# Optimization experiments

Measured on AMD Instinct MI355X. Metric: run time of the kernel, lower is better.

Reference implementation:

```python
import jax, jax.numpy as jnp
import numpy as np

N_AGENTS = 32
STATE_DIM = 2048
EMBED = 64
BS, T = 64, 32


def setup_inputs() -> dict:
    key = jax.random.key(0)
    ks = jax.random.split(key, 12)
    def lin(k, fan_in, fan_out):
        return jax.random.normal(k, (fan_in, fan_out), dtype=jnp.float32) / np.sqrt(fan_in)
    return {
        "agent_qs": jax.random.normal(ks[0], (BS, T, N_AGENTS), dtype=jnp.float32),
        "states": jax.random.normal(ks[1], (BS, T, STATE_DIM), dtype=jnp.float32),
        "Ww1": lin(ks[2], STATE_DIM, EMBED * N_AGENTS),
        "bw1": jnp.zeros((EMBED * N_AGENTS,), jnp.float32),
        "Wwf": lin(ks[3], STATE_DIM, EMBED),
        "bwf": jnp.zeros((EMBED,), jnp.float32),
        "Wb1": lin(ks[4], STATE_DIM, EMBED),
        "bb1": jnp.zeros((EMBED,), jnp.float32),
        "Wv1": lin(ks[5], STATE_DIM, EMBED),
        "bv1": jnp.zeros((EMBED,), jnp.float32),
        "Wv2": lin(ks[6], EMBED, 1),
        "bv2": jnp.zeros((1,), jnp.float32),
    }


def _mix(qs, st, Ww1, bw1, Wwf, bwf, Wb1, bb1, Wv1, bv1, Wv2, bv2):
    # qs: [B,1,A], st: [B,S] -> q_tot [B]
    w1 = jnp.abs(st @ Ww1 + bw1).reshape(-1, N_AGENTS, EMBED)          # [B,A,E]
    b1 = (st @ Wb1 + bb1)[:, None, :]                                   # [B,1,E]
    hidden = jax.nn.elu(jnp.einsum('bia,bae->bie', qs, w1) + b1)        # [B,1,E]
    w_final = jnp.abs(st @ Wwf + bwf)                                   # [B,E]
    v = jax.nn.relu(st @ Wv1 + bv1) @ Wv2 + bv2                         # [B,1]
    y = jnp.einsum('bie,be->bi', hidden, w_final) + v                   # [B,1]
    return y[:, 0]


def reference(agent_qs, states, Ww1, bw1, Wwf, bwf, Wb1, bb1, Wv1, bv1, Wv2, bv2):
    bs = agent_qs.shape[0]
    st = states.reshape(-1, STATE_DIM)                   # [B,S]
    qs = agent_qs.reshape(-1, 1, N_AGENTS)               # [B,1,A]
    B = st.shape[0]
    params = (Ww1, bw1, Wwf, bwf, Wb1, bb1, Wv1, bv1, Wv2, bv2)

    # --- wc_calculate (fully detached) ---
    q_tot = _mix(qs, st, *params)                        # [B]
    dim2 = STATE_DIM // N_AGENTS
    st3 = st.reshape(B, N_AGENTS, dim2)
    mask = 1.0 - jnp.eye(N_AGENTS, dtype=st.dtype)       # [A,A]: row i zeros agent-i chunk
    masked = (st3[None, :, :, :] * mask[:, None, :, None]).reshape(N_AGENTS * B, STATE_DIM)
    qs_rep = jnp.broadcast_to(qs[None], (N_AGENTS, B, 1, N_AGENTS)).reshape(N_AGENTS * B, 1, N_AGENTS)
    q1 = _mix(qs_rep, masked, *params).reshape(N_AGENTS, B)
    wc = jnp.abs(q_tot[None, :] - q1).T                  # [B,A]
    wc = wc / jnp.maximum(jnp.linalg.norm(wc, axis=1, keepdims=True), 1e-12)
    wc = jax.lax.stop_gradient(wc)[:, None, :]           # [B,1,A]

    # --- final mix with importance-weighted qs ---
    q_tot_final = _mix(qs * wc, st, *params)             # [B]
    return q_tot_final.reshape(bs, -1, 1)
```

## Files before the change

### kernel.cpp

```cpp
#include <hip/hip_runtime.h>
#include <math.h>
#include <stdint.h>

#define NA 32
#define SD 2048
#define BT 2048
#define NFRG 144

typedef float floatx4 __attribute__((ext_vector_type(4)));
typedef short bf16x8  __attribute__((ext_vector_type(8)));

__device__ __forceinline__ unsigned short f2bf(float f) {
    union { float f; uint32_t u; } v; v.f = f;
    uint32_t r = v.u + 0x7FFFu + ((v.u >> 16) & 1u);
    return (unsigned short)(r >> 16);
}

__device__ __forceinline__ void stage16(const void* g, void* l) {
    __builtin_amdgcn_global_load_lds(
        (const __attribute__((address_space(1))) void*)g,
        (__attribute__((address_space(3))) void*)l,
        16, 0, 0);
}


__global__ __launch_bounds__(256) void k0_ast(const float* __restrict__ st,
                                              unsigned short* __restrict__ stA) {
    const int t  = threadIdx.x;
    const int kc = blockIdx.x * 4 + (t >> 6);
    const int bt = blockIdx.y;
    const int l  = t & 63;
    const int quad = l >> 4, l16 = l & 15;
    const float* src = st + (size_t)(bt * 16 + l16) * SD + kc * 32 + quad * 8;
    float4 v0 = *(const float4*)(src);
    float4 v1 = *(const float4*)(src + 4);
    ushort4 o0, o1;
    o0.x = f2bf(v0.x); o0.y = f2bf(v0.y); o0.z = f2bf(v0.z); o0.w = f2bf(v0.w);
    o1.x = f2bf(v1.x); o1.y = f2bf(v1.y); o1.z = f2bf(v1.z); o1.w = f2bf(v1.w);
    unsigned short* dst = stA + ((size_t)bt * 64 + kc) * 512 + l * 8;
    *(ushort4*)(dst)     = o0;
    *(ushort4*)(dst + 4) = o1;
}

__global__ __launch_bounds__(256) void k0_wswz(const float* __restrict__ Ww1,
                                               const float* __restrict__ Wwf,
                                               const float* __restrict__ Wb1,
                                               const float* __restrict__ Wv1,
                                               unsigned short* __restrict__ Wswz) {
    const int t = threadIdx.x;
    const int i = blockIdx.y;
    const int f = blockIdx.x * 2 + (t >> 7);
    const int h = (t >> 6) & 1;
    const int l = t & 63;
    const int quad = l >> 4, l16 = l & 15;
    const int n = f * 16 + l16;

    const float* src; int ld, nr = 0;
    if (f < 128)      { src = Ww1; ld = 2048; nr = n; }
    else if (f < 132) { src = Wwf; ld = 64;   nr = n - 2048; }
    else if (f < 136) { src = Wb1; ld = 64;   nr = n - 2112; }
    else if (f < 140) { src = Wv1; ld = 64;   nr = n - 2176; }
    else              { src = nullptr; ld = 64; }

    const int k0 = i * 64 + h * 32 + quad * 8;
    unsigned short vals[8];
    #pragma unroll
    for (int j = 0; j < 8; j++)
        vals[j] = src ? f2bf(src[(size_t)(k0 + j) * ld + nr]) : (unsigned short)0;

    unsigned short* dst = Wswz + (((size_t)i * NFRG + f) * 2 + h) * 512 + l * 8;
    ushort4 o0 = {vals[0], vals[1], vals[2], vals[3]};
    ushort4 o1 = {vals[4], vals[5], vals[6], vals[7]};
    *(ushort4*)(dst)     = o0;
    *(ushort4*)(dst + 4) = o1;
}

__global__ void k0_bias(const float* __restrict__ bw1, const float* __restrict__ bwf,
                        const float* __restrict__ bb1, const float* __restrict__ bv1,
                        float* __restrict__ bcat) {
    int n = blockIdx.x * 256 + threadIdx.x;
    if (n >= NFRG * 16) return;
    float v = 0.f;
    if (n < 2048)      v = bw1[n];
    else if (n < 2112) v = bwf[n - 2048];
    else if (n < 2176) v = bb1[n - 2112];
    else if (n < 2240) v = bv1[n - 2176];
    bcat[n] = v;
}

__global__ __launch_bounds__(256) void k1_gemm(const unsigned short* __restrict__ stA,
                                               const unsigned short* __restrict__ Wswz,
                                               const float* __restrict__ bcat,
                                               float* __restrict__ Ycn)
{
    const int t = threadIdx.x;
    const int m0t = blockIdx.x * 4;
    const int n0f = blockIdx.y * 8;
    const int wid = t >> 6, lane = t & 63;
    const int wm = wid & 1, wn = wid >> 1;
    const int l16 = lane & 15;

    floatx4 acc[2][4];
    #pragma unroll
    for (int i = 0; i < 2; i++)
        #pragma unroll
        for (int j = 0; j < 4; j++) acc[i][j] = (floatx4)0.f;

    const unsigned short* Ap0 = stA + ((size_t)(m0t + wm * 2 + 0) * 64) * 512 + lane * 8;
    const unsigned short* Ap1 = stA + ((size_t)(m0t + wm * 2 + 1) * 64) * 512 + lane * 8;
    const unsigned short* Bbase = Wswz + ((size_t)(n0f + wn * 4) * 2) * 512 + lane * 8;

    bf16x8 a0c = *(const bf16x8*)(Ap0);
    bf16x8 a1c = *(const bf16x8*)(Ap1);
    bf16x8 bc[4];
    #pragma unroll
    for (int nf = 0; nf < 4; nf++)
        bc[nf] = *(const bf16x8*)(Bbase + (size_t)nf * 1024);

    for (int kc = 0; kc < 64; kc++) {
        bf16x8 a0n, a1n, bn[4];
        if (kc < 63) {
            const int kn = kc + 1;
            a0n = *(const bf16x8*)(Ap0 + (size_t)kn * 512);
            a1n = *(const bf16x8*)(Ap1 + (size_t)kn * 512);
            const unsigned short* Bp =
                Bbase + ((size_t)(kn >> 1) * NFRG * 2 + (kn & 1)) * 512;
            #pragma unroll
            for (int nf = 0; nf < 4; nf++)
                bn[nf] = *(const bf16x8*)(Bp + (size_t)nf * 1024);
        }
        #pragma unroll
        for (int nf = 0; nf < 4; nf++) {
            acc[0][nf] = __builtin_amdgcn_mfma_f32_16x16x32_bf16(a0c, bc[nf], acc[0][nf], 0, 0, 0);
            acc[1][nf] = __builtin_amdgcn_mfma_f32_16x16x32_bf16(a1c, bc[nf], acc[1][nf], 0, 0, 0);
        }
        a0c = a0n; a1c = a1n;
        #pragma unroll
        for (int nf = 0; nf < 4; nf++) bc[nf] = bn[nf];
    }

    #pragma unroll
    for (int mf = 0; mf < 2; mf++)
        #pragma unroll
        for (int nf = 0; nf < 4; nf++) {
            const int f  = n0f + wn * 4 + nf;
            const int bt = m0t + wm * 2 + mf;
            const float bias = bcat[f * 16 + l16];
            floatx4 o;
            #pragma unroll
            for (int r = 0; r < 4; r++) o[r] = -(acc[mf][nf][r] + bias);
            *(floatx4*)(Ycn + ((size_t)bt * NFRG + f) * 256 + lane * 4) = o;
        }
}

__global__ __launch_bounds__(256) void k3_q1(
    const unsigned short* __restrict__ stA, const float* __restrict__ qs,
    const unsigned short* __restrict__ Wswz, const float* __restrict__ Wv2,
    const float* __restrict__ bv2, const float* __restrict__ Ycn,
    float* __restrict__ q1)
{
    const int p   = blockIdx.x;
    const int btg = blockIdx.y;
    const int t = threadIdx.x;
    const int w = t >> 6, lane = t & 63;
    const int bt = btg * 4 + w;
    const int quad = lane >> 4, l16 = lane & 15;
    const int im[2] = { p, p + 16 };

    __shared__ unsigned short Wl[2][2][4][2][512];
    __shared__ float qs_s[4][16][33];

    {
        int b = lane >> 2, a0 = (lane & 3) * 8;
        const float* src = qs + (size_t)(bt * 16 + b) * NA + a0;
        #pragma unroll
        for (int u = 0; u < 8; u++) qs_s[w][b][a0 + u] = src[u];
    }

    bf16x8 A0[2], A1[2];
    #pragma unroll
    for (int m = 0; m < 2; m++) {
        A0[m] = *(const bf16x8*)(stA + ((size_t)bt * 64 + 2 * im[m] + 0) * 512 + lane * 8);
        A1[m] = *(const bf16x8*)(stA + ((size_t)bt * 64 + 2 * im[m] + 1) * 512 + lane * 8);
    }

    const float* Yb = Ycn + (size_t)bt * NFRG * 256 + lane * 4;

    auto stage = [&](int fg, int buf) {
        #pragma unroll
        for (int j = 0; j < 4; j++) {
            const int c  = w * 4 + j;
            const int m  = c >> 3;
            const int nf = (c >> 1) & 3;
            const int h  = c & 1;
            const unsigned short* g = Wswz
                + ((size_t)(im[m] * NFRG + fg * 4 + nf) * 2 + h) * 512 + lane * 8;
            stage16(g, &Wl[buf][m][nf][h][0]);
        }
    };

    floatx4 yv[4], yn[4], acc[2][4];

    auto wmfma = [&](int buf) {
        #pragma unroll
        for (int m = 0; m < 2; m++)
            #pragma unroll
            for (int nf = 0; nf < 4; nf++) {
                bf16x8 w0 = *(const bf16x8*)&Wl[buf][m][nf][0][lane * 8];
                bf16x8 w1 = *(const bf16x8*)&Wl[buf][m][nf][1][lane * 8];
                floatx4 a = __builtin_amdgcn_mfma_f32_16x16x32_bf16(A0[m], w0, yv[nf], 0, 0, 0);
                acc[m][nf] = __builtin_amdgcn_mfma_f32_16x16x32_bf16(A1[m], w1, a, 0, 0, 0);
            }
    };

    floatx4 hid[2][4];
    #pragma unroll
    for (int m = 0; m < 2; m++)
        #pragma unroll
        for (int nf = 0; nf < 4; nf++) hid[m][nf] = (floatx4)0.f;

    stage(0, 0);
    #pragma unroll
    for (int nf = 0; nf < 4; nf++) yv[nf] = *(const floatx4*)(Yb + (size_t)nf * 256);
    __syncthreads();

    for (int fg = 0; fg < 32; fg++) {
        const int cur = fg & 1;
        stage(fg + 1, cur ^ 1);
        {
            const float* yp = Yb + (size_t)(fg + 1) * 4 * 256;
            #pragma unroll
            for (int nf = 0; nf < 4; nf++) yn[nf] = *(const floatx4*)(yp + (size_t)nf * 256);
        }
        wmfma(cur);
        float qv[4];
        #pragma unroll
        for (int r = 0; r < 4; r++) qv[r] = qs_s[w][quad * 4 + r][fg];
        #pragma unroll
        for (int m = 0; m < 2; m++)
            #pragma unroll
            for (int nf = 0; nf < 4; nf++)
                #pragma unroll
                for (int r = 0; r < 4; r++)
                    hid[m][nf][r] += qv[r] * fabsf(acc[m][nf][r]);
        #pragma unroll
        for (int nf = 0; nf < 4; nf++) yv[nf] = yn[nf];
        __syncthreads();
    }

    floatx4 wff[2][4], b1f[2][4], vacc[2];

    {
        stage(33, 1);
        {
            const float* yp = Yb + (size_t)33 * 4 * 256;
            #pragma unroll
            for (int nf = 0; nf < 4; nf++) yn[nf] = *(const floatx4*)(yp + (size_t)nf * 256);
        }
        wmfma(0);
        #pragma unroll
        for (int m = 0; m < 2; m++)
            #pragma unroll
            for (int nf = 0; nf < 4; nf++)
                #pragma unroll
                for (int r = 0; r < 4; r++) wff[m][nf][r] = fabsf(acc[m][nf][r]);
        #pragma unroll
        for (int nf = 0; nf < 4; nf++) yv[nf] = yn[nf];
        __syncthreads();
    }
    {
        stage(34, 0);
        {
            const float* yp = Yb + (size_t)34 * 4 * 256;
            #pragma unroll
            for (int nf = 0; nf < 4; nf++) yn[nf] = *(const floatx4*)(yp + (size_t)nf * 256);
        }
        wmfma(1);
        #pragma unroll
        for (int m = 0; m < 2; m++)
            #pragma unroll
            for (int nf = 0; nf < 4; nf++)
                #pragma unroll
                for (int r = 0; r < 4; r++) b1f[m][nf][r] = -acc[m][nf][r];
        #pragma unroll
        for (int nf = 0; nf < 4; nf++) yv[nf] = yn[nf];
        __syncthreads();
    }
    {
        wmfma(0);
        float wv2f[4];
        #pragma unroll
        for (int nf = 0; nf < 4; nf++) wv2f[nf] = Wv2[nf * 16 + l16];
        #pragma unroll
        for (int m = 0; m < 2; m++) {
            vacc[m] = (floatx4)0.f;
            #pragma unroll
            for (int nf = 0; nf < 4; nf++)
                #pragma unroll
                for (int r = 0; r < 4; r++)
                    vacc[m][r] += fmaxf(-acc[m][nf][r], 0.f) * wv2f[nf];
        }
    }

    const float bv2v = bv2[0];
    #pragma unroll
    for (int m = 0; m < 2; m++)
        #pragma unroll
        for (int r = 0; r < 4; r++) {
            float s = vacc[m][r];
            #pragma unroll
            for (int nf = 0; nf < 4; nf++) {
                float h = hid[m][nf][r] + b1f[m][nf][r];
                h = h > 0.f ? h : expm1f(h);
                s += h * wff[m][nf][r];
            }
            s += __shfl_xor(s, 1); s += __shfl_xor(s, 2);
            s += __shfl_xor(s, 4); s += __shfl_xor(s, 8);
            if (l16 == 0) q1[(size_t)im[m] * BT + bt * 16 + quad * 4 + r] = s + bv2v;
        }
}

__global__ __launch_bounds__(256) void k4_final(
    const float* __restrict__ qs, const float* __restrict__ Ycn,
    const float* __restrict__ q1, const float* __restrict__ Wv2,
    const float* __restrict__ bv2, float* __restrict__ out)
{
    const int bt = blockIdx.x;
    __shared__ float qs_s[16][33];
    __shared__ float qw_s[16][33];
    __shared__ float hidp[4][16][64];
    __shared__ float wfb[16][64], b1b[16][64], vb[16][64];
    __shared__ float qt[16];

    const int t = threadIdx.x, w = t >> 6, lane = t & 63;
    const int quad = lane >> 4, l16 = lane & 15;
    const float bv2v = bv2[0];

    {
        int l = t * 2;
        float2 v = *(const float2*)&qs[(size_t)(bt * 16 + (l >> 5)) * NA + (l & 31)];
        qs_s[l >> 5][(l & 31) + 0] = v.x;
        qs_s[l >> 5][(l & 31) + 1] = v.y;
    }
    __syncthreads();

    const float* Yb = Ycn + (size_t)bt * NFRG * 256;

    floatx4 hid[4];
    #pragma unroll
    for (int nf = 0; nf < 4; nf++) hid[nf] = (floatx4)0.f;
    for (int ia = 0; ia < 8; ia++) {
        const int a = w * 8 + ia;
        const float* yp = Yb + (size_t)(a * 4) * 256 + lane * 4;
        float qv[4];
        #pragma unroll
        for (int r = 0; r < 4; r++) qv[r] = qs_s[quad * 4 + r][a];
        #pragma unroll
        for (int nf = 0; nf < 4; nf++) {
            floatx4 c = *(const floatx4*)(yp + nf * 256);
            #pragma unroll
            for (int r = 0; r < 4; r++) hid[nf][r] += qv[r] * fabsf(c[r]);
        }
    }
    #pragma unroll
    for (int nf = 0; nf < 4; nf++)
        #pragma unroll
        for (int r = 0; r < 4; r++)
            hidp[w][quad * 4 + r][nf * 16 + l16] = hid[nf][r];

    #pragma unroll
    for (int fi = 0; fi < 3; fi++) {
        const int nft = w * 3 + fi;
        floatx4 c = *(const floatx4*)(Yb + (size_t)(128 + nft) * 256 + lane * 4);
        const int e = (nft & 3) * 16 + l16;
        #pragma unroll
        for (int r = 0; r < 4; r++) {
            int b = quad * 4 + r;
            if (nft < 4)      wfb[b][e] = fabsf(c[r]);
            else if (nft < 8) b1b[b][e] = -c[r];
            else              vb[b][e]  = fmaxf(-c[r], 0.f) * Wv2[e];
        }
    }
    __syncthreads();

    #pragma unroll
    for (int bb = 0; bb < 4; bb++) {
        int b = w * 4 + bb;
        float h = hidp[0][b][lane] + hidp[1][b][lane]
                + hidp[2][b][lane] + hidp[3][b][lane] + b1b[b][lane];
        h = h > 0.f ? h : expm1f(h);
        float val = h * wfb[b][lane] + vb[b][lane];
        #pragma unroll
        for (int off = 32; off > 0; off >>= 1) val += __shfl_xor(val, off);
        if (lane == 0) qt[b] = val + bv2v;
    }
    __syncthreads();

    {
        const int rr = w * 4 + quad;
        float qtv = qt[rr];
        float d0 = fabsf(qtv - q1[(size_t)(2 * l16 + 0) * BT + bt * 16 + rr]);
        float d1 = fabsf(qtv - q1[(size_t)(2 * l16 + 1) * BT + bt * 16 + rr]);
        float ss = d0 * d0 + d1 * d1;
        ss += __shfl_xor(ss, 1); ss += __shfl_xor(ss, 2);
        ss += __shfl_xor(ss, 4); ss += __shfl_xor(ss, 8);
        float inv = 1.f / fmaxf(sqrtf(ss), 1e-12f);
        qw_s[rr][2 * l16 + 0] = qs_s[rr][2 * l16 + 0] * d0 * inv;
        qw_s[rr][2 * l16 + 1] = qs_s[rr][2 * l16 + 1] * d1 * inv;
    }
    __syncthreads();

    floatx4 hid2[4];
    #pragma unroll
    for (int nf = 0; nf < 4; nf++) hid2[nf] = (floatx4)0.f;
    for (int ia = 0; ia < 8; ia++) {
        const int a = w * 8 + ia;
        const float* yp = Yb + (size_t)(a * 4) * 256 + lane * 4;
        float qv[4];
        #pragma unroll
        for (int r = 0; r < 4; r++) qv[r] = qw_s[quad * 4 + r][a];
        #pragma unroll
        for (int nf = 0; nf < 4; nf++) {
            floatx4 c = *(const floatx4*)(yp + nf * 256);
            #pragma unroll
            for (int r = 0; r < 4; r++) hid2[nf][r] += qv[r] * fabsf(c[r]);
        }
    }
    #pragma unroll
    for (int nf = 0; nf < 4; nf++)
        #pragma unroll
        for (int r = 0; r < 4; r++)
            hidp[w][quad * 4 + r][nf * 16 + l16] = hid2[nf][r];
    __syncthreads();

    #pragma unroll
    for (int bb = 0; bb < 4; bb++) {
        int b = w * 4 + bb;
        float h = hidp[0][b][lane] + hidp[1][b][lane]
                + hidp[2][b][lane] + hidp[3][b][lane] + b1b[b][lane];
        h = h > 0.f ? h : expm1f(h);
        float val = h * wfb[b][lane] + vb[b][lane];
        #pragma unroll
        for (int off = 32; off > 0; off >>= 1) val += __shfl_xor(val, off);
        if (lane == 0) out[bt * 16 + b] = val + bv2v;
    }
}

extern "C" void kernel_launch(void* const* d_in, const int* in_sizes, int n_in,
                              void* d_out, int out_size, void* d_ws, size_t ws_size,
                              hipStream_t stream) {
    const float* qs  = (const float*)d_in[0];
    const float* st  = (const float*)d_in[1];
    const float* Ww1 = (const float*)d_in[2];
    const float* bw1 = (const float*)d_in[3];
    const float* Wwf = (const float*)d_in[4];
    const float* bwf = (const float*)d_in[5];
    const float* Wb1 = (const float*)d_in[6];
    const float* bb1 = (const float*)d_in[7];
    const float* Wv1 = (const float*)d_in[8];
    const float* bv1 = (const float*)d_in[9];
    const float* Wv2 = (const float*)d_in[10];
    const float* bv2 = (const float*)d_in[11];
    float* out = (float*)d_out;

    float* Ycn           = (float*)d_ws;
    unsigned short* stA  = (unsigned short*)(Ycn + (size_t)128 * NFRG * 256);
    unsigned short* Wswz = stA + (size_t)SD * SD;
    float* bcat          = (float*)(Wswz + (size_t)32 * NFRG * 1024);
    float* q1v           = bcat + NFRG * 16;

    k0_ast <<<dim3(16, 128), 256, 0, stream>>>(st, stA);
    k0_wswz<<<dim3(NFRG / 2, 32), 256, 0, stream>>>(Ww1, Wwf, Wb1, Wv1, Wswz);
    k0_bias<<<(NFRG * 16 + 255) / 256, 256, 0, stream>>>(bw1, bwf, bb1, bv1, bcat);

    k1_gemm<<<dim3(BT / 64, NFRG / 8), 256, 0, stream>>>(stA, Wswz, bcat, Ycn);
    k3_q1  <<<dim3(16, 32), 256, 0, stream>>>(stA, qs, Wswz, Wv2, bv2, Ycn, q1v);
    k4_final<<<BT / 16, 256, 0, stream>>>(qs, Ycn, q1v, Wv2, bv2, out);
}
```

Measured before the change: 193.3 us.

## Deepen weight staging pipeline with manual vmcnt waits and split barriers

```diff
diff --git a/kernel.cpp b/kernel.cpp
--- a/kernel.cpp
+++ b/kernel.cpp
@@ -193,9 +193,9 @@
             const int m  = c >> 3;
             const int nf = (c >> 1) & 3;
             const int h  = c & 1;
-            const unsigned short* g = Wswz
+            const unsigned short* gp = Wswz
                 + ((size_t)(im[m] * NFRG + fg * 4 + nf) * 2 + h) * 512 + lane * 8;
-            stage16(g, &Wl[buf][m][nf][h][0]);
+            stage16(gp, &Wl[buf][m][nf][h][0]);
         }
     };
 
@@ -213,93 +213,77 @@
             }
     };
 
-    floatx4 hid[2][4];
-    #pragma unroll
-    for (int m = 0; m < 2; m++)
+    floatx4 hid[2][4], wff[2][4], b1f[2][4], vacc[2];
+    #pragma unroll
+    for (int m = 0; m < 2; m++) {
+        vacc[m] = (floatx4)0.f;
         #pragma unroll
         for (int nf = 0; nf < 4; nf++) hid[m][nf] = (floatx4)0.f;
+    }
 
     stage(0, 0);
     #pragma unroll
     for (int nf = 0; nf < 4; nf++) yv[nf] = *(const floatx4*)(Yb + (size_t)nf * 256);
-    __syncthreads();
-
-    for (int fg = 0; fg < 32; fg++) {
-        const int cur = fg & 1;
-        stage(fg + 1, cur ^ 1);
-        {
+    stage(1, 1);
+    asm volatile("s_waitcnt vmcnt(4)" ::: "memory");
+    __builtin_amdgcn_sched_barrier(0);
+    __builtin_amdgcn_s_barrier();
+
+    for (int fg = 0; fg < 35; fg++) {
+        const int buf = fg & 1;
+        if (fg < 34) {
             const float* yp = Yb + (size_t)(fg + 1) * 4 * 256;
             #pragma unroll
             for (int nf = 0; nf < 4; nf++) yn[nf] = *(const floatx4*)(yp + (size_t)nf * 256);
         }
-        wmfma(cur);
-        float qv[4];
-        #pragma unroll
-        for (int r = 0; r < 4; r++) qv[r] = qs_s[w][quad * 4 + r][fg];
-        #pragma unroll
-        for (int m = 0; m < 2; m++)
-            #pragma unroll
-            for (int nf = 0; nf < 4; nf++)
+        wmfma(buf);
+        if (fg < 32) {
+            float qv[4];
+            #pragma unroll
+            for (int r = 0; r < 4; r++) qv[r] = qs_s[w][quad * 4 + r][fg];
+            #pragma unroll
+            for (int m = 0; m < 2; m++)
                 #pragma unroll
-                for (int r = 0; r < 4; r++)
-                    hid[m][nf][r] += qv[r] * fabsf(acc[m][nf][r]);
+                for (int nf = 0; nf < 4; nf++)
+                    #pragma unroll
+                    for (int r = 0; r < 4; r++)
+                        hid[m][nf][r] += qv[r] * fabsf(acc[m][nf][r]);
+        } else if (fg == 32) {
+            #pragma unroll
+            for (int m = 0; m < 2; m++)
+                #pragma unroll
+                for (int nf = 0; nf < 4; nf++)
+                    #pragma unroll
+                    for (int r = 0; r < 4; r++) wff[m][nf][r] = fabsf(acc[m][nf][r]);
+        } else if (fg == 33) {
+            #pragma unroll
+            for (int m = 0; m < 2; m++)
+                #pragma unroll
+                for (int nf = 0; nf < 4; nf++)
+                    #pragma unroll
+                    for (int r = 0; r < 4; r++) b1f[m][nf][r] = -acc[m][nf][r];
+        } else {
+            float wv2f[4];
+            #pragma unroll
+            for (int nf = 0; nf < 4; nf++) wv2f[nf] = Wv2[nf * 16 + l16];
+            #pragma unroll
+            for (int m = 0; m < 2; m++)
+                #pragma unroll
+                for (int nf = 0; nf < 4; nf++)
+                    #pragma unroll
+                    for (int r = 0; r < 4; r++)
+                        vacc[m][r] += fmaxf(-acc[m][nf][r], 0.f) * wv2f[nf];
+        }
+        __builtin_amdgcn_sched_barrier(0);
+        __builtin_amdgcn_s_barrier();
+        __builtin_amdgcn_sched_barrier(0);
+        if (fg <= 33) stage(fg + 2, buf);
+        asm volatile("s_waitcnt vmcnt(4)" ::: "memory");
+        __builtin_amdgcn_sched_barrier(0);
+        __builtin_amdgcn_s_barrier();
+        __builtin_amdgcn_sched_barrier(0);
         #pragma unroll
         for (int nf = 0; nf < 4; nf++) yv[nf] = yn[nf];
-        __syncthreads();
-    }
-
-    floatx4 wff[2][4], b1f[2][4], vacc[2];
-
-    {
-        stage(33, 1);
-        {
-            const float* yp = Yb + (size_t)33 * 4 * 256;
-            #pragma unroll
-            for (int nf = 0; nf < 4; nf++) yn[nf] = *(const floatx4*)(yp + (size_t)nf * 256);
-        }
-        wmfma(0);
-        #pragma unroll
-        for (int m = 0; m < 2; m++)
-            #pragma unroll
-            for (int nf = 0; nf < 4; nf++)
-                #pragma unroll
-                for (int r = 0; r < 4; r++) wff[m][nf][r] = fabsf(acc[m][nf][r]);
-        #pragma unroll
-        for (int nf = 0; nf < 4; nf++) yv[nf] = yn[nf];
-        __syncthreads();
-    }
-    {
-        stage(34, 0);
-        {
-            const float* yp = Yb + (size_t)34 * 4 * 256;
-            #pragma unroll
-            for (int nf = 0; nf < 4; nf++) yn[nf] = *(const floatx4*)(yp + (size_t)nf * 256);
-        }
-        wmfma(1);
-        #pragma unroll
-        for (int m = 0; m < 2; m++)
-            #pragma unroll
-            for (int nf = 0; nf < 4; nf++)
-                #pragma unroll
-                for (int r = 0; r < 4; r++) b1f[m][nf][r] = -acc[m][nf][r];
-        #pragma unroll
-        for (int nf = 0; nf < 4; nf++) yv[nf] = yn[nf];
-        __syncthreads();
-    }
-    {
-        wmfma(0);
-        float wv2f[4];
-        #pragma unroll
-        for (int nf = 0; nf < 4; nf++) wv2f[nf] = Wv2[nf * 16 + l16];
-        #pragma unroll
-        for (int m = 0; m < 2; m++) {
-            vacc[m] = (floatx4)0.f;
-            #pragma unroll
-            for (int nf = 0; nf < 4; nf++)
-                #pragma unroll
-                for (int r = 0; r < 4; r++)
-                    vacc[m][r] += fmaxf(-acc[m][nf][r], 0.f) * wv2f[nf];
-        }
     }
 
     const float bv2v = bv2[0];
```

After: 223.4 us. +15.6%, slower.

## Stage GEMM tiles in LDS with double buffering and fold bias launch

Applied to the files above, without the earlier changes.

```diff
diff --git a/kernel.cpp b/kernel.cpp
--- a/kernel.cpp
+++ b/kernel.cpp
@@ -75,22 +75,12 @@
     *(ushort4*)(dst + 4) = o1;
 }
 
-__global__ void k0_bias(const float* __restrict__ bw1, const float* __restrict__ bwf,
-                        const float* __restrict__ bb1, const float* __restrict__ bv1,
-                        float* __restrict__ bcat) {
-    int n = blockIdx.x * 256 + threadIdx.x;
-    if (n >= NFRG * 16) return;
-    float v = 0.f;
-    if (n < 2048)      v = bw1[n];
-    else if (n < 2112) v = bwf[n - 2048];
-    else if (n < 2176) v = bb1[n - 2112];
-    else if (n < 2240) v = bv1[n - 2176];
-    bcat[n] = v;
-}
-
 __global__ __launch_bounds__(256) void k1_gemm(const unsigned short* __restrict__ stA,
                                                const unsigned short* __restrict__ Wswz,
-                                               const float* __restrict__ bcat,
+                                               const float* __restrict__ bw1,
+                                               const float* __restrict__ bwf,
+                                               const float* __restrict__ bb1,
+                                               const float* __restrict__ bv1,
                                                float* __restrict__ Ycn)
 {
     const int t = threadIdx.x;
@@ -100,43 +90,55 @@
     const int wm = wid & 1, wn = wid >> 1;
     const int l16 = lane & 15;
 
+    __shared__ unsigned short As[2][2][4][512];
+    __shared__ unsigned short Bs[2][2][8][512];
+
     floatx4 acc[2][4];
     #pragma unroll
     for (int i = 0; i < 2; i++)
         #pragma unroll
         for (int j = 0; j < 4; j++) acc[i][j] = (floatx4)0.f;
 
-    const unsigned short* Ap0 = stA + ((size_t)(m0t + wm * 2 + 0) * 64) * 512 + lane * 8;
-    const unsigned short* Ap1 = stA + ((size_t)(m0t + wm * 2 + 1) * 64) * 512 + lane * 8;
-    const unsigned short* Bbase = Wswz + ((size_t)(n0f + wn * 4) * 2) * 512 + lane * 8;
-
-    bf16x8 a0c = *(const bf16x8*)(Ap0);
-    bf16x8 a1c = *(const bf16x8*)(Ap1);
-    bf16x8 bc[4];
-    #pragma unroll
-    for (int nf = 0; nf < 4; nf++)
-        bc[nf] = *(const bf16x8*)(Bbase + (size_t)nf * 1024);
-
-    for (int kc = 0; kc < 64; kc++) {
-        bf16x8 a0n, a1n, bn[4];
-        if (kc < 63) {
-            const int kn = kc + 1;
-            a0n = *(const bf16x8*)(Ap0 + (size_t)kn * 512);
-            a1n = *(const bf16x8*)(Ap1 + (size_t)kn * 512);
-            const unsigned short* Bp =
-                Bbase + ((size_t)(kn >> 1) * NFRG * 2 + (kn & 1)) * 512;
+    auto stage = [&](int it, int buf) {
+        #pragma unroll
+        for (int j = 0; j < 6; j++) {
+            const int c   = wid * 6 + j;
+            const int kk  = c / 12;
+            const int rem = c % 12;
+            if (rem < 4) {
+                const unsigned short* gp = stA
+                    + ((size_t)(m0t + rem) * 64 + (it * 2 + kk)) * 512 + lane * 8;
+                stage16(gp, &As[buf][kk][rem][0]);
+            } else {
+                const int f = rem - 4;
+                const unsigned short* gp = Wswz
+                    + (((size_t)it * NFRG + (n0f + f)) * 2 + kk) * 512 + lane * 8;
+                stage16(gp, &Bs[buf][kk][f][0]);
+            }
+        }
+    };
+
+    stage(0, 0);
+    __syncthreads();
+
+    for (int it = 0; it < 32; it++) {
+        const int buf = it & 1;
+        if (it < 31) stage(it + 1, buf ^ 1);
+        #pragma unroll
+        for (int kk = 0; kk < 2; kk++) {
+            bf16x8 a0 = *(const bf16x8*)&As[buf][kk][wm * 2 + 0][lane * 8];
+            bf16x8 a1 = *(const bf16x8*)&As[buf][kk][wm * 2 + 1][lane * 8];
+            bf16x8 b[4];
             #pragma unroll
             for (int nf = 0; nf < 4; nf++)
-                bn[nf] = *(const bf16x8*)(Bp + (size_t)nf * 1024);
-        }
-        #pragma unroll
-        for (int nf = 0; nf < 4; nf++) {
-            acc[0][nf] = __builtin_amdgcn_mfma_f32_16x16x32_bf16(a0c, bc[nf], acc[0][nf], 0, 0, 0);
-            acc[1][nf] = __builtin_amdgcn_mfma_f32_16x16x32_bf16(a1c, bc[nf], acc[1][nf], 0, 0, 0);
-        }
-        a0c = a0n; a1c = a1n;
-        #pragma unroll
-        for (int nf = 0; nf < 4; nf++) bc[nf] = bn[nf];
+                b[nf] = *(const bf16x8*)&Bs[buf][kk][wn * 4 + nf][lane * 8];
+            #pragma unroll
+            for (int nf = 0; nf < 4; nf++) {
+                acc[0][nf] = __builtin_amdgcn_mfma_f32_16x16x32_bf16(a0, b[nf], acc[0][nf], 0, 0, 0);
+                acc[1][nf] = __builtin_amdgcn_mfma_f32_16x16x32_bf16(a1, b[nf], acc[1][nf], 0, 0, 0);
+            }
+        }
+        __syncthreads();
     }
 
     #pragma unroll
@@ -145,7 +147,13 @@
         for (int nf = 0; nf < 4; nf++) {
             const int f  = n0f + wn * 4 + nf;
             const int bt = m0t + wm * 2 + mf;
-            const float bias = bcat[f * 16 + l16];
+            const int n  = f * 16 + l16;
+            float bias;
+            if (f < 128)      bias = bw1[n];
+            else if (f < 132) bias = bwf[n - 2048];
+            else if (f < 136) bias = bb1[n - 2112];
+            else if (f < 140) bias = bv1[n - 2176];
+            else              bias = 0.f;
             floatx4 o;
             #pragma unroll
             for (int r = 0; r < 4; r++) o[r] = -(acc[mf][nf][r] + bias);
@@ -471,9 +479,8 @@
 
     k0_ast <<<dim3(16, 128), 256, 0, stream>>>(st, stA);
     k0_wswz<<<dim3(NFRG / 2, 32), 256, 0, stream>>>(Ww1, Wwf, Wb1, Wv1, Wswz);
-    k0_bias<<<(NFRG * 16 + 255) / 256, 256, 0, stream>>>(bw1, bwf, bb1, bv1, bcat);
-
-    k1_gemm<<<dim3(BT / 64, NFRG / 8), 256, 0, stream>>>(stA, Wswz, bcat, Ycn);
+
+    k1_gemm<<<dim3(BT / 64, NFRG / 8), 256, 0, stream>>>(stA, Wswz, bw1, bwf, bb1, bv1, Ycn);
     k3_q1  <<<dim3(16, 32), 256, 0, stream>>>(stA, qs, Wswz, Wv2, bv2, Ycn, q1v);
     k4_final<<<BT / 16, 256, 0, stream>>>(qs, Ycn, q1v, Wv2, bv2, out);
 }
```

New measurement: 182.7 us. 1.06x faster.
